# Performance work log

Measured on AMD Instinct MI355X. Metric: run time of the kernel, lower is better.

Reference implementation:

```python
import jax, jax.numpy as jnp
import numpy as np

# Fixed production-scale dims (equal-size graphs -> no ragged padding needed)
B, NPG, C, H, L, FFN, NC = 16, 512, 128, 8, 4, 512, 4
D = C // H          # head dim = 16
T = NPG + 1         # +1 virtual graph token
EPG = 8192          # edges per graph (avg degree 16)
E = B * EPG


def _ln(x, g, b, eps=1e-5):
    m = x.mean(-1, keepdims=True)
    v = ((x - m) ** 2).mean(-1, keepdims=True)
    return (x - m) * jax.lax.rsqrt(v + eps) * g + b


def setup_inputs() -> dict:
    key = jax.random.key(0)
    ks = jax.random.split(key, 24)
    N = B * NPG
    node_feats = jax.random.normal(ks[0], (N, 3), jnp.float32)
    # intra-graph edges: local endpoints + per-graph node offset (matches batch_ptr math)
    local = jax.random.randint(ks[1], (2, B, EPG), 0, NPG)
    offs = (jnp.arange(B) * NPG)[None, :, None]
    edge_index = (local + offs).reshape(2, E)
    edge_attr = jax.random.randint(ks[2], (E,), 0, 10)

    def nrm(k, shape, scale=0.02):
        return jax.random.normal(k, shape, jnp.float32) * scale

    params = {
        "W_node": nrm(ks[3], (3, C), 0.3), "b_node": jnp.zeros((C,), jnp.float32),
        "graph_token": nrm(ks[4], (C,), 1.0),
        "edge_bias_table": nrm(ks[5], (11, H), 0.1).at[0].set(0.0),  # padding_idx=0
        "in_deg_emb": nrm(ks[6], (512, C)).at[0].set(0.0),           # padding_idx=0
        "out_deg_emb": nrm(ks[7], (512, C)).at[0].set(0.0),
        "vnode_bias": nrm(ks[8], (H,), 1.0),
        "Wq": nrm(ks[9], (L, C, C)), "bq": jnp.zeros((L, C), jnp.float32),
        "Wk": nrm(ks[10], (L, C, C)), "bk": jnp.zeros((L, C), jnp.float32),
        "Wv": nrm(ks[11], (L, C, C)), "bv": jnp.zeros((L, C), jnp.float32),
        "Wo": nrm(ks[12], (L, C, C)), "bo": jnp.zeros((L, C), jnp.float32),
        "ln1_g": jnp.ones((L, C), jnp.float32), "ln1_b": jnp.zeros((L, C), jnp.float32),
        "ln2_g": jnp.ones((L, C), jnp.float32), "ln2_b": jnp.zeros((L, C), jnp.float32),
        "W1": nrm(ks[13], (L, C, FFN)), "b1": jnp.zeros((L, FFN), jnp.float32),
        "W2": nrm(ks[14], (L, FFN, C)), "b2": jnp.zeros((L, C), jnp.float32),
        "normf_g": jnp.ones((C,), jnp.float32), "normf_b": jnp.zeros((C,), jnp.float32),
        "Wc1": nrm(ks[15], (C, C // 2)), "bc1": jnp.zeros((C // 2,), jnp.float32),
        "Wc2": nrm(ks[16], (C // 2, NC)), "bc2": jnp.zeros((NC,), jnp.float32),
    }
    return {"node_feats": node_feats, "edge_index": edge_index,
            "edge_attr": edge_attr, "num_graphs": B, **params}


def reference(node_feats, W_node, b_node, graph_token, edge_bias_table,
              in_deg_emb, out_deg_emb, vnode_bias,
              Wq, bq, Wk, bk, Wv, bv, Wo, bo,
              ln1_g, ln1_b, ln2_g, ln2_b, W1, b1, W2, b2,
              normf_g, normf_b, Wc1, bc1, Wc2, bc2,
              edge_index, edge_attr, num_graphs):
    N = node_feats.shape[0]
    npg = N // num_graphs
    t = npg + 1
    src, dst = edge_index[0], edge_index[1]
    # degree encoders (scatter_add of ones == segment_sum)
    in_deg = jnp.clip(jax.ops.segment_sum(jnp.ones_like(dst), dst, num_segments=N), 0, 511)
    out_deg = jnp.clip(jax.ops.segment_sum(jnp.ones_like(src), src, num_segments=N), 0, 511)
    x_enc = node_feats @ W_node + b_node + in_deg_emb[in_deg] + out_deg_emb[out_deg]
    # equal-size graphs with sorted batch ids -> padding loop is a reshape, mask all-False
    x = jnp.concatenate(
        [jnp.broadcast_to(graph_token, (num_graphs, 1, C)),
         x_enc.reshape(num_graphs, npg, C)], axis=1)  # [B, T, C]
    # attention bias: vnode row/col + scattered edge-attr embeddings
    bias = jnp.zeros((num_graphs, H, t, t), jnp.float32)
    bias = bias.at[:, :, 0, :].set(vnode_bias[None, :, None])
    bias = bias.at[:, :, :, 0].set(vnode_bias[None, :, None])
    eb = edge_bias_table[jnp.clip(edge_attr, 0, 9) + 1]  # [E, H]
    g = src // npg
    sl = src - g * npg + 1
    dl = dst - g * npg + 1
    bias = bias.at[g, :, sl, dl].add(eb)  # duplicate edges accumulate (scatter_add)
    scale = 1.0 / np.sqrt(D).astype(np.float32)
    for l in range(L):  # key_padding_mask is all-False here -> masked_fill is a no-op
        h = _ln(x, ln1_g[l], ln1_b[l])
        q = (h @ Wq[l] + bq[l]).reshape(num_graphs, t, H, D)
        k = (h @ Wk[l] + bk[l]).reshape(num_graphs, t, H, D)
        v = (h @ Wv[l] + bv[l]).reshape(num_graphs, t, H, D)
        scores = jnp.einsum('bthd,bshd->bhts', q, k) * scale + bias
        attn = jax.nn.softmax(scores, axis=-1)
        o = jnp.einsum('bhts,bshd->bthd', attn, v).reshape(num_graphs, t, C)
        x = x + o @ Wo[l] + bo[l]
        h2 = _ln(x, ln2_g[l], ln2_b[l])
        x = x + jax.nn.gelu(h2 @ W1[l] + b1[l], approximate=False) @ W2[l] + b2[l]
    x = _ln(x, normf_g, normf_b)
    gr = x[:, 0, :]  # virtual-node readout
    return jax.nn.gelu(gr @ Wc1 + bc1, approximate=False) @ Wc2 + bc2
```

## Files before the change

### kernel.cpp

```cpp
#include <hip/hip_runtime.h>
#include <hip/hip_bf16.h>

#define BB 16
#define NPG 512
#define CC 128
#define HH 8
#define LL 4
#define FFN 512
#define NCLS 4
#define DD 16
#define TT 513
#define EE 131072
#define NNODES 8192
#define ROWS (BB * TT)
#define ECAP 64
#define SP 544
#define BPAD 544

static constexpr size_t XROWS = (size_t)BB * TT;
static constexpr size_t XSZ   = XROWS * CC;
static constexpr size_t VTSZ  = (size_t)BB * HH * DD * SP;
static constexpr size_t BIASSZ = (size_t)BB * HH * 513 * BPAD;

typedef unsigned short ushort_t;
typedef __attribute__((ext_vector_type(8))) short short8;
typedef __attribute__((ext_vector_type(4))) float floatx4;

__device__ __forceinline__ float gelu_exact(float v) {
    return 0.5f * v * (1.0f + erff(v * 0.70710678118654752440f));
}
__device__ __forceinline__ ushort_t f2bf(float f) {
    union { float f; unsigned u; } c; c.f = f;
    unsigned u = c.u;
    return (ushort_t)((u + 0x7FFFu + ((u >> 16) & 1u)) >> 16);
}
__device__ __forceinline__ float bf2f(ushort_t u) {
    union { unsigned u; float f; } c; c.u = ((unsigned)u) << 16; return c.f;
}
__device__ __forceinline__ int swz(int row, int col, int stride) {
    int kb = col >> 3;
    return row * stride + (((kb ^ (row & 7)) << 3) | (col & 7));
}

__device__ __forceinline__ void qkv_stage8(const ushort_t* hs,
                                           const ushort_t* Wtq, const float* bq_,
                                           const ushort_t* Wtk, const float* bk_,
                                           const ushort_t* Wtv, const float* bv_,
                                           ushort_t* qb, ushort_t* kb, ushort_t* vt,
                                           int b, int t0, int wave, int lq, int quad) {
    const short* hsS = (const short*)hs;
    int c = wave * 16 + lq;
    const short* Ws[3] = {(const short*)Wtq, (const short*)Wtk, (const short*)Wtv};
    const float* bs[3] = {bq_, bk_, bv_};
    size_t rB = (size_t)c * CC;

    #pragma unroll
    for (int m = 0; m < 3; ++m) {
        const short* W = Ws[m];
        floatx4 a0 = {0.f,0.f,0.f,0.f};
        #pragma unroll
        for (int k0 = 0; k0 < CC; k0 += 32) {
            short8 af = *(const short8*)(hsS + swz(lq, k0 + quad * 8, 128));
            short8 b0 = *(const short8*)(W + rB + k0 + quad * 8);
            a0 = __builtin_amdgcn_mfma_f32_16x16x32_bf16(af, b0, a0, 0, 0, 0);
        }
        float bv0 = bs[m][c];
        #pragma unroll
        for (int rg = 0; rg < 4; ++rg) {
            int t = t0 + quad * 4 + rg;
            if (t >= TT) continue;
            size_t r = (size_t)b * TT + t;
            float v0 = a0[rg] + bv0;
            if (m == 0) {
                qb[r * CC + c] = f2bf(v0 * 0.25f);
            } else if (m == 1) {
                kb[r * CC + c] = f2bf(v0);
            } else {
                vt[((size_t)(b * HH + wave) * DD + lq) * SP + t] = f2bf(v0);
            }
        }
    }
}

__global__ __launch_bounds__(256) void deg_csr_tr_kernel(const int* __restrict__ ei,
                                                         const int* __restrict__ ea,
                                                         int* __restrict__ deg_in,
                                                         int* __restrict__ deg_out,
                                                         int* __restrict__ cnt,
                                                         int* __restrict__ ebuf,
                                                         const float* __restrict__ Wq,
                                                         const float* __restrict__ Wk,
                                                         const float* __restrict__ Wv,
                                                         const float* __restrict__ Wo,
                                                         const float* __restrict__ W1,
                                                         const float* __restrict__ W2,
                                                         ushort_t* __restrict__ wtqkvo,
                                                         ushort_t* __restrict__ wt1,
                                                         ushort_t* __restrict__ wt2) {
    int bid = blockIdx.x;
    int tid = threadIdx.x;
    if (bid < 512) {
        int e = bid * 256 + tid;
        int src = ei[e], dst = ei[EE + e];
        atomicAdd(&deg_out[src], 1);
        atomicAdd(&deg_in[dst], 1);
        int g = src >> 9;
        int sl = src - (g << 9) + 1;
        int dl = dst - (g << 9) + 1;
        int a = ea[e];
        a = (a < 0) ? 0 : (a > 9 ? 9 : a);
        a += 1;
        int row = g * TT + sl;
        int pos = atomicAdd(&cnt[row], 1);
        if (pos < ECAP) ebuf[(size_t)row * ECAP + pos] = dl | (a << 16);
        return;
    }
    int z = bid - 512;
    const float* src; ushort_t* dst; int K, N, tile;
    if (z < 64) {
        int zz = z >> 2; tile = z & 3;
        int k = zz >> 2, l = zz & 3;
        const float* s4[4] = {Wq, Wk, Wv, Wo};
        src = s4[k] + (size_t)l * CC * CC;
        dst = wtqkvo + (size_t)(k * 4 + l) * 16384;
        K = CC; N = CC;
    } else if (z < 128) {
        int l = (z - 64) >> 4; tile = (z - 64) & 15;
        src = W1 + (size_t)l * CC * FFN;
        dst = wt1 + (size_t)l * 65536;
        K = CC; N = FFN;
    } else {
        int l = (z - 128) >> 4; tile = (z - 128) & 15;
        src = W2 + (size_t)l * FFN * CC;
        dst = wt2 + (size_t)l * 65536;
        K = FFN; N = CC;
    }
    int tilesN = N >> 6;
    int k0 = (tile / tilesN) << 6;
    int n0 = (tile - (tile / tilesN) * tilesN) << 6;
    __shared__ float t[64][65];
    int c = tid & 63, rb = tid >> 6;
    #pragma unroll
    for (int kk = 0; kk < 64; kk += 4)
        t[kk + rb][c] = src[(size_t)(k0 + kk + rb) * N + n0 + c];
    __syncthreads();
    #pragma unroll
    for (int nn = 0; nn < 64; nn += 4)
        dst[(size_t)(n0 + nn + rb) * K + k0 + c] = f2bf(t[c][nn + rb]);
}

__global__ __launch_bounds__(512) void pre_kernel(const float* __restrict__ nf,
                                                  const float* __restrict__ Wn,
                                                  const float* __restrict__ bn,
                                                  const float* __restrict__ gt,
                                                  const float* __restrict__ ide,
                                                  const float* __restrict__ ode,
                                                  const int* __restrict__ deg_in,
                                                  const int* __restrict__ deg_out,
                                                  const float* __restrict__ ln1g_,
                                                  const float* __restrict__ ln1b_,
                                                  const ushort_t* __restrict__ wtqkvo,
                                                  const float* __restrict__ bq_,
                                                  const float* __restrict__ bk_,
                                                  const float* __restrict__ bv_,
                                                  float* __restrict__ x_,
                                                  ushort_t* __restrict__ qb,
                                                  ushort_t* __restrict__ kb,
                                                  ushort_t* __restrict__ vt,
                                                  const int* __restrict__ cnt,
                                                  const int* __restrict__ ebuf,
                                                  const float* __restrict__ ebt,
                                                  ushort_t* __restrict__ bias_d) {
    int bid = blockIdx.x;
    int tid = threadIdx.x;
    __shared__ __align__(16) char parena[17408];

    if (bid >= 528) {
        int z = bid - 528;
        int b = z / 513;
        int sl = z - b * 513;
        float* row8 = (float*)parena;
        for (int i = tid; i < 8 * BPAD / 4; i += 512)
            ((float4*)row8)[i] = make_float4(0.f, 0.f, 0.f, 0.f);
        __syncthreads();
        int crow = b * TT + sl;
        int cn = min(cnt[crow], ECAP);
        int h = tid & 7;
        for (int j = tid >> 3; j < cn; j += 64) {
            int e = ebuf[(size_t)crow * ECAP + j];
            atomicAdd(&row8[h * BPAD + (e & 0xFFFF)], ebt[(e >> 16) * 8 + h]);
        }
        __syncthreads();
        #pragma unroll
        for (int hh = 0; hh < HH; ++hh) {
            size_t base = ((size_t)(b * HH + hh) * 513 + sl) * BPAD;
            for (int s = tid; s < BPAD; s += 512)
                bias_d[base + s] = f2bf(row8[hh * BPAD + s]);
        }
        return;
    }

    int b = bid / 33, qt = bid - b * 33;
    int t0 = qt * 16;
    int wave = tid >> 6, lane = tid & 63, lq = lane & 15, quad = lane >> 4;
    ushort_t* hs = (ushort_t*)parena;
    auto sred = (float (*)[16][2])(parena + 4096);

    int c = wave * 16 + lq;
    float w0[4];
    #pragma unroll
    for (int rg = 0; rg < 4; ++rg) {
        int t = t0 + quad * 4 + rg;
        int tc = min(t, TT - 1);
        float v0;
        if (tc == 0) {
            v0 = gt[c];
        } else {
            int i = b * NPG + tc - 1;
            float f0 = nf[i*3+0], f1 = nf[i*3+1], f2 = nf[i*3+2];
            v0 = bn[c] + f0*Wn[0*CC + c] + f1*Wn[1*CC + c] + f2*Wn[2*CC + c];
            int di = min(deg_in[i], 511);
            int dq = min(deg_out[i], 511);
            v0 += ide[(size_t)di * CC + c] + ode[(size_t)dq * CC + c];
        }
        if (t < TT) x_[((size_t)b * TT + t) * CC + c] = v0;
        w0[rg] = v0;
    }
    #pragma unroll
    for (int rg = 0; rg < 4; ++rg) {
        float s1 = w0[rg];
        float s2 = w0[rg] * w0[rg];
        #pragma unroll
        for (int m = 1; m < 16; m <<= 1) {
            s1 += __shfl_xor(s1, m, 64);
            s2 += __shfl_xor(s2, m, 64);
        }
        if (lq == 0) { sred[wave][quad*4+rg][0] = s1; sred[wave][quad*4+rg][1] = s2; }
    }
    __syncthreads();
    float g0 = ln1g_[c], lb0 = ln1b_[c];
    #pragma unroll
    for (int rg = 0; rg < 4; ++rg) {
        int row = quad * 4 + rg;
        float S1 = 0.f, S2 = 0.f;
        #pragma unroll
        for (int w = 0; w < 8; ++w) { S1 += sred[w][row][0]; S2 += sred[w][row][1]; }
        float mn = S1 * (1.0f/CC);
        float var = S2 * (1.0f/CC) - mn * mn;
        float rs = rsqrtf(var + 1e-5f);
        hs[swz(row, c, 128)] = f2bf((w0[rg] - mn) * rs * g0 + lb0);
    }
    __syncthreads();
    qkv_stage8(hs, wtqkvo, bq_,
               wtqkvo + (size_t)4 * 16384, bk_,
               wtqkvo + (size_t)8 * 16384, bv_,
               qb, kb, vt, b, t0, wave, lq, quad);
}

__global__ __launch_bounds__(512, 4) void layer_kernel(const ushort_t* __restrict__ qbr,
                                                       const ushort_t* __restrict__ kbr,
                                                       const ushort_t* __restrict__ vtr,
                                                       const ushort_t* __restrict__ bias_d,
                                                       const float* __restrict__ vnode,
                                                       const ushort_t* __restrict__ WtO,
                                                       const float* __restrict__ bo_,
                                                       const float* __restrict__ ln2g_,
                                                       const float* __restrict__ ln2b_,
                                                       const ushort_t* __restrict__ Wt1_,
                                                       const float* __restrict__ b1_,
                                                       const ushort_t* __restrict__ Wt2_,
                                                       const float* __restrict__ b2_,
                                                       const float* __restrict__ ln1g_,
                                                       const float* __restrict__ ln1b_,
                                                       const ushort_t* __restrict__ Wtq,
                                                       const float* __restrict__ bq_,
                                                       const ushort_t* __restrict__ Wtk,
                                                       const float* __restrict__ bk_,
                                                       const ushort_t* __restrict__ Wtv,
                                                       const float* __restrict__ bv_,
                                                       const float* __restrict__ nfg,
                                                       const float* __restrict__ nfb,
                                                       const float* __restrict__ Wc1,
                                                       const float* __restrict__ bc1,
                                                       const float* __restrict__ Wc2,
                                                       const float* __restrict__ bc2,
                                                       float* __restrict__ x_,
                                                       ushort_t* __restrict__ qbw,
                                                       ushort_t* __restrict__ kbw,
                                                       ushort_t* __restrict__ vtw,
                                                       float* __restrict__ out,
                                                       int doQKV) {
    int qt = blockIdx.x, b = blockIdx.y;
    int tid = threadIdx.x;
    int wave = tid >> 6, lane = tid & 63, lq = lane & 15, quad = lane >> 4;

    __shared__ __align__(16) char smem[20480];
    ushort_t* hs = (ushort_t*)smem;
    ushort_t* ms = (ushort_t*)(smem + 4096);
    __shared__ __align__(16) ushort_t obs[16 * 128];
    __shared__ float sred[8][16][2];

    {
        int h = wave;
        int qg = qt * 16 + lq;
        int qr = min(qg, TT - 1);
        short8 z8 = {0,0,0,0,0,0,0,0};
        short8 qf = z8;
        if (quad < 2)
            qf = *(const short8*)(qbr + ((size_t)(b * TT + qr)) * CC + h * DD + quad * 8);
        float vn = vnode[h];
        const short* kbS = (const short*)kbr;
        const short* vtS = (const short*)(vtr + (size_t)(b * HH + h) * DD * SP);
        const ushort_t* brow = bias_d + ((size_t)(b * HH + h) * 513 + qr) * BPAD;

        short8 af0c = z8, af1c = z8, vfc;
        {
            int kr0 = min(b * TT + lq, (int)XROWS - 1);
            int kr1 = min(b * TT + 16 + lq, (int)XROWS - 1);
            if (quad < 2) {
                af0c = *(const short8*)(kbS + (size_t)kr0 * CC + h * DD + quad * 8);
                af1c = *(const short8*)(kbS + (size_t)kr1 * CC + h * DD + quad * 8);
            }
            vfc = *(const short8*)(vtS + (size_t)lq * SP + quad * 8);
        }
        uint2 bi0c = *(const uint2*)(brow + quad * 4);
        uint2 bi1c = *(const uint2*)(brow + 16 + quad * 4);

        floatx4 oacc = {0.f, 0.f, 0.f, 0.f};
        float lsum = 0.f;

        for (int sp = 0; sp < 17; ++sp) {
            int spn = sp + 1;
            short8 af0n = z8, af1n = z8, vfn = z8;
            uint2 bi0n = make_uint2(0u, 0u), bi1n = make_uint2(0u, 0u);
            if (spn < 17) {
                int st0 = spn * 2, st1 = st0 + 1;
                int kr0 = min(b * TT + st0 * 16 + lq, (int)XROWS - 1);
                int kr1 = min(b * TT + st1 * 16 + lq, (int)XROWS - 1);
                if (quad < 2) {
                    af0n = *(const short8*)(kbS + (size_t)kr0 * CC + h * DD + quad * 8);
                    af1n = *(const short8*)(kbS + (size_t)kr1 * CC + h * DD + quad * 8);
                }
                vfn = *(const short8*)(vtS + (size_t)lq * SP + spn * 32 + quad * 8);
                bi0n = *(const uint2*)(brow + spn * 32 + quad * 4);
                bi1n = *(const uint2*)(brow + spn * 32 + 16 + quad * 4);
            }
            float vadd = ((sp == 0) & (quad == 0) & (qg > 0)) ? vn : 0.f;

            unsigned pw[2][2];
            #pragma unroll
            for (int t = 0; t < 2; ++t) {
                int st = sp * 2 + t;
                floatx4 cc4 = __builtin_amdgcn_mfma_f32_16x16x32_bf16(
                    t ? af1c : af0c, qf, (floatx4){0.f, 0.f, 0.f, 0.f}, 0, 0, 0);
                uint2 bi = t ? bi1c : bi0c;
                float pr[4];
                #pragma unroll
                for (int rg = 0; rg < 4; ++rg) {
                    int s = st * 16 + quad * 4 + rg;
                    unsigned bw = (rg < 2) ? bi.x : bi.y;
                    float bb = bf2f((rg & 1) ? (ushort_t)(bw >> 16) : (ushort_t)(bw & 0xFFFFu));
                    if (t == 0 && rg == 0) bb += vadd;
                    float p = 0.f;
                    if (s < TT) p = __expf(cc4[rg] + bb);
                    lsum += p;
                    pr[rg] = p;
                }
                pw[t][0] = (unsigned)f2bf(pr[0]) | ((unsigned)f2bf(pr[1]) << 16);
                pw[t][1] = (unsigned)f2bf(pr[2]) | ((unsigned)f2bf(pr[3]) << 16);
            }
            int srcA = lq + (((2 * quad) & 3) << 4);
            int srcB = lq + (((2 * quad + 1) & 3) << 4);
            int a00 = __shfl((int)pw[0][0], srcA, 64);
            int a01 = __shfl((int)pw[0][1], srcA, 64);
            int a10 = __shfl((int)pw[1][0], srcA, 64);
            int a11 = __shfl((int)pw[1][1], srcA, 64);
            int b00 = __shfl((int)pw[0][0], srcB, 64);
            int b01 = __shfl((int)pw[0][1], srcB, 64);
            int b10 = __shfl((int)pw[1][0], srcB, 64);
            int b11 = __shfl((int)pw[1][1], srcB, 64);
            union { int u[4]; short8 s8; } pu;
            bool lo = quad < 2;
            pu.u[0] = lo ? a00 : a10;
            pu.u[1] = lo ? a01 : a11;
            pu.u[2] = lo ? b00 : b10;
            pu.u[3] = lo ? b01 : b11;
            oacc = __builtin_amdgcn_mfma_f32_16x16x32_bf16(vfc, pu.s8, oacc, 0, 0, 0);

            af0c = af0n; af1c = af1n; vfc = vfn; bi0c = bi0n; bi1c = bi1n;
        }

        lsum += __shfl_xor(lsum, 16, 64);
        lsum += __shfl_xor(lsum, 32, 64);
        #pragma unroll
        for (int rg = 0; rg < 4; ++rg)
            obs[swz(lq, h * DD + quad * 4 + rg, 128)] = f2bf(oacc[rg] / lsum);
    }
    __syncthreads();

    int t0 = qt * 16;
    int c = wave * 16 + lq;
    float vv0[4];
    const short* obsS = (const short*)obs;

    {
        const short* W = (const short*)WtO;
        size_t rB = (size_t)c * CC;
        floatx4 a0 = {0.f,0.f,0.f,0.f};
        #pragma unroll
        for (int k0 = 0; k0 < CC; k0 += 32) {
            short8 af = *(const short8*)(obsS + swz(lq, k0 + quad * 8, 128));
            short8 b0 = *(const short8*)(W + rB + k0 + quad * 8);
            a0 = __builtin_amdgcn_mfma_f32_16x16x32_bf16(af, b0, a0, 0, 0, 0);
        }
        float bv0 = bo_[c];
        #pragma unroll
        for (int rg = 0; rg < 4; ++rg) {
            int t = t0 + quad * 4 + rg;
            size_t rc = (size_t)b * TT + min(t, TT - 1);
            vv0[rg] = a0[rg] + bv0 + x_[rc * CC + c];
        }
        #pragma unroll
        for (int rg = 0; rg < 4; ++rg) {
            float s1 = vv0[rg];
            float s2 = vv0[rg] * vv0[rg];
            #pragma unroll
            for (int m = 1; m < 16; m <<= 1) {
                s1 += __shfl_xor(s1, m, 64);
                s2 += __shfl_xor(s2, m, 64);
            }
            if (lq == 0) { sred[wave][quad*4+rg][0] = s1; sred[wave][quad*4+rg][1] = s2; }
        }
        __syncthreads();
        float g0 = ln2g_[c], lb0 = ln2b_[c];
        #pragma unroll
        for (int rg = 0; rg < 4; ++rg) {
            int row = quad * 4 + rg;
            float S1 = 0.f, S2 = 0.f;
            #pragma unroll
            for (int w = 0; w < 8; ++w) { S1 += sred[w][row][0]; S2 += sred[w][row][1]; }
            float mn = S1 * (1.0f/CC);
            float var = S2 * (1.0f/CC) - mn * mn;
            float rs = rsqrtf(var + 1e-5f);
            hs[swz(row, c, 128)] = f2bf((vv0[rg] - mn) * rs * g0 + lb0);
        }
    }
    __syncthreads();

    {
        const short* hsS = (const short*)hs;
        const short* W = (const short*)Wt1_;
        #pragma unroll
        for (int nt = 0; nt < 4; ++nt) {
            int n = wave * 64 + nt * 16;
            size_t rB = (size_t)(n + lq) * CC;
            floatx4 a0 = {0.f,0.f,0.f,0.f};
            #pragma unroll
            for (int k0 = 0; k0 < CC; k0 += 32) {
                short8 af = *(const short8*)(hsS + swz(lq, k0 + quad * 8, 128));
                short8 b0 = *(const short8*)(W + rB + k0 + quad * 8);
                a0 = __builtin_amdgcn_mfma_f32_16x16x32_bf16(af, b0, a0, 0, 0, 0);
            }
            float bb0 = b1_[n + lq];
            #pragma unroll
            for (int rg = 0; rg < 4; ++rg)
                ms[swz(quad * 4 + rg, n + lq, 512)] = f2bf(gelu_exact(a0[rg] + bb0));
        }
    }
    __syncthreads();

    float w0[4];
    {
        const short* msS = (const short*)ms;
        const short* W = (const short*)Wt2_;
        size_t rB = (size_t)c * FFN;
        floatx4 a0 = {0.f,0.f,0.f,0.f};
        #pragma unroll 8
        for (int k0 = 0; k0 < FFN; k0 += 32) {
            short8 af = *(const short8*)(msS + swz(lq, k0 + quad * 8, 512));
            short8 b0 = *(const short8*)(W + rB + k0 + quad * 8);
            a0 = __builtin_amdgcn_mfma_f32_16x16x32_bf16(af, b0, a0, 0, 0, 0);
        }
        float bv0 = b2_[c];
        #pragma unroll
        for (int rg = 0; rg < 4; ++rg) {
            int t = t0 + quad * 4 + rg;
            w0[rg] = a0[rg] + bv0 + vv0[rg];
            if (t < TT) x_[((size_t)b * TT + t) * CC + c] = w0[rg];
        }
    }

    if (doQKV) {
        #pragma unroll
        for (int rg = 0; rg < 4; ++rg) {
            float s1 = w0[rg];
            float s2 = w0[rg] * w0[rg];
            #pragma unroll
            for (int m = 1; m < 16; m <<= 1) {
                s1 += __shfl_xor(s1, m, 64);
                s2 += __shfl_xor(s2, m, 64);
            }
            if (lq == 0) { sred[wave][quad*4+rg][0] = s1; sred[wave][quad*4+rg][1] = s2; }
        }
        __syncthreads();
        float g0 = ln1g_[c], lb0 = ln1b_[c];
        #pragma unroll
        for (int rg = 0; rg < 4; ++rg) {
            int row = quad * 4 + rg;
            float S1 = 0.f, S2 = 0.f;
            #pragma unroll
            for (int w = 0; w < 8; ++w) { S1 += sred[w][row][0]; S2 += sred[w][row][1]; }
            float mn = S1 * (1.0f/CC);
            float var = S2 * (1.0f/CC) - mn * mn;
            float rs = rsqrtf(var + 1e-5f);
            hs[swz(row, c, 128)] = f2bf((w0[rg] - mn) * rs * g0 + lb0);
        }
        __syncthreads();
        qkv_stage8(hs, Wtq, bq_, Wtk, bk_, Wtv, bv_, qbw, kbw, vtw, b, t0, wave, lq, quad);
        return;
    }

    if (qt != 0) return;

    __syncthreads();
    float* hrow = (float*)ms;
    float* xfs  = hrow + CC;
    float* c1s  = xfs + CC;
    float* red  = c1s + 64;
    if (quad == 0) hrow[c] = w0[0];
    __syncthreads();

    {
        int ct = tid;
        float v = 0.f, s1 = 0.f, s2 = 0.f;
        if (ct < CC) { v = hrow[ct]; s1 = v; s2 = v * v; }
        #pragma unroll
        for (int m = 32; m >= 1; m >>= 1) {
            s1 += __shfl_xor(s1, m, 64);
            s2 += __shfl_xor(s2, m, 64);
        }
        int w = ct >> 6;
        if (ct < CC && (ct & 63) == 0) { red[w*2] = s1; red[w*2+1] = s2; }
        __syncthreads();
        if (ct < CC) {
            float S1 = red[0] + red[2], S2 = red[1] + red[3];
            float mn = S1 * (1.0f/CC);
            float var = S2 * (1.0f/CC) - mn * mn;
            float rs = rsqrtf(var + 1e-5f);
            xfs[ct] = (v - mn) * rs * nfg[ct] + nfb[ct];
        }
        __syncthreads();
        if (ct < 64) {
            float acc = bc1[ct];
            #pragma unroll 4
            for (int k = 0; k < CC; ++k) acc = fmaf(xfs[k], Wc1[(size_t)k * 64 + ct], acc);
            c1s[ct] = gelu_exact(acc);
        }
        __syncthreads();
        if (ct < NCLS) {
            float acc = bc2[ct];
            #pragma unroll 4
            for (int j = 0; j < 64; ++j) acc = fmaf(c1s[j], Wc2[(size_t)j * NCLS + ct], acc);
            out[(size_t)b * NCLS + ct] = acc;
        }
    }
}

extern "C" void kernel_launch(void* const* d_in, const int* in_sizes, int n_in,
                              void* d_out, int out_size, void* d_ws, size_t ws_size,
                              hipStream_t stream) {
    const float* node_feats = (const float*)d_in[0];
    const int*   edge_index = (const int*)d_in[1];
    const int*   edge_attr  = (const int*)d_in[2];
    const float* W_node  = (const float*)d_in[4];
    const float* b_node  = (const float*)d_in[5];
    const float* g_token = (const float*)d_in[6];
    const float* ebt     = (const float*)d_in[7];
    const float* ide     = (const float*)d_in[8];
    const float* ode     = (const float*)d_in[9];
    const float* vnode   = (const float*)d_in[10];
    const float* Wq = (const float*)d_in[11];
    const float* bq = (const float*)d_in[12];
    const float* Wk = (const float*)d_in[13];
    const float* bk = (const float*)d_in[14];
    const float* Wv = (const float*)d_in[15];
    const float* bv = (const float*)d_in[16];
    const float* Wo = (const float*)d_in[17];
    const float* bo = (const float*)d_in[18];
    const float* ln1g = (const float*)d_in[19];
    const float* ln1b = (const float*)d_in[20];
    const float* ln2g = (const float*)d_in[21];
    const float* ln2b = (const float*)d_in[22];
    const float* W1 = (const float*)d_in[23];
    const float* b1 = (const float*)d_in[24];
    const float* W2 = (const float*)d_in[25];
    const float* b2 = (const float*)d_in[26];
    const float* nfg = (const float*)d_in[27];
    const float* nfb = (const float*)d_in[28];
    const float* Wc1 = (const float*)d_in[29];
    const float* bc1 = (const float*)d_in[30];
    const float* Wc2 = (const float*)d_in[31];
    const float* bc2 = (const float*)d_in[32];
    float* out = (float*)d_out;

    char* base = (char*)d_ws;
    float* x      = (float*)base;     base += XSZ * 4;
    ushort_t* qb0 = (ushort_t*)base;  base += XSZ * 2;
    ushort_t* kb0 = (ushort_t*)base;  base += XSZ * 2;
    ushort_t* vt0 = (ushort_t*)base;  base += VTSZ * 2;
    ushort_t* qb1 = (ushort_t*)base;  base += XSZ * 2;
    ushort_t* kb1 = (ushort_t*)base;  base += XSZ * 2;
    ushort_t* vt1 = (ushort_t*)base;  base += VTSZ * 2;
    ushort_t* wtqkvo = (ushort_t*)base; base += (size_t)16 * 16384 * 2;
    ushort_t* wt1 = (ushort_t*)base;  base += (size_t)4 * 65536 * 2;
    ushort_t* wt2 = (ushort_t*)base;  base += (size_t)4 * 65536 * 2;
    ushort_t* bias_d = (ushort_t*)base; base += BIASSZ * 2;
    int* deg_in  = (int*)base;        base += NNODES * 4;
    int* deg_out = (int*)base;        base += NNODES * 4;
    int* cnt     = (int*)base;        base += (size_t)ROWS * 4;
    int* ebuf    = (int*)base;        base += (size_t)ROWS * ECAP * 4;

    ushort_t* qbs[2] = {qb0, qb1};
    ushort_t* kbs[2] = {kb0, kb1};
    ushort_t* vts[2] = {vt0, vt1};

    hipMemsetAsync(deg_in, 0, (size_t)(2 * NNODES + ROWS) * 4, stream);
    deg_csr_tr_kernel<<<512 + 192, 256, 0, stream>>>(
        edge_index, edge_attr, deg_in, deg_out, cnt, ebuf,
        Wq, Wk, Wv, Wo, W1, W2, wtqkvo, wt1, wt2);

    pre_kernel<<<528 + 8208, 512, 0, stream>>>(
        node_feats, W_node, b_node, g_token, ide, ode, deg_in, deg_out,
        ln1g, ln1b, wtqkvo, bq, bk, bv, x, qb0, kb0, vt0,
        cnt, ebuf, ebt, bias_d);

    for (int l = 0; l < LL; ++l) {
        int rd = l & 1, wr = rd ^ 1;
        int ln = (l + 1) % LL;
        layer_kernel<<<dim3(33, BB), 512, 0, stream>>>(
            qbs[rd], kbs[rd], vts[rd], bias_d, vnode,
            wtqkvo + (size_t)(12 + l)*16384, bo + l*CC,
            ln2g + l*CC, ln2b + l*CC,
            wt1 + (size_t)l*65536, b1 + l*FFN,
            wt2 + (size_t)l*65536, b2 + l*CC,
            ln1g + ln*CC, ln1b + ln*CC,
            wtqkvo + (size_t)(0 + ln)*16384, bq + ln*CC,
            wtqkvo + (size_t)(4 + ln)*16384, bk + ln*CC,
            wtqkvo + (size_t)(8 + ln)*16384, bv + ln*CC,
            nfg, nfb, Wc1, bc1, Wc2, bc2,
            x, qbs[wr], kbs[wr], vts[wr], out,
            (l < LL-1) ? 1 : 0);
    }
}
```

Measured before the change: 464.8 us.

## Build attention bias on the fly from per-row edge lists instead of dense bias

Drops the dense bf16 bias tensor (B*H*513*544) that pre_kernel materialized and each layer re-read. Each layer_kernel block now loads the per-query-row edge lists and the edge bias table into shared memory. For each 64-column window it scatters those edges into a per-wave LDS strip with atomicAdd before computing the softmax. This removes a large global write plus four full reads of the bias, at the cost of repeating the scatter work in every layer, extra LDS use (which may limit occupancy) and LDS atomics inside the inner attention loop.

```diff
diff --git a/kernel.cpp b/kernel.cpp
--- a/kernel.cpp
+++ b/kernel.cpp
@@ -15,12 +15,11 @@
 #define ROWS (BB * TT)
 #define ECAP 64
 #define SP 544
-#define BPAD 544
+#define ESTR 68
 
 static constexpr size_t XROWS = (size_t)BB * TT;
 static constexpr size_t XSZ   = XROWS * CC;
 static constexpr size_t VTSZ  = (size_t)BB * HH * DD * SP;
-static constexpr size_t BIASSZ = (size_t)BB * HH * 513 * BPAD;
 
 typedef unsigned short ushort_t;
 typedef __attribute__((ext_vector_type(8))) short short8;
@@ -33,9 +32,6 @@
     union { float f; unsigned u; } c; c.f = f;
     unsigned u = c.u;
     return (ushort_t)((u + 0x7FFFu + ((u >> 16) & 1u)) >> 16);
-}
-__device__ __forceinline__ float bf2f(ushort_t u) {
-    union { unsigned u; float f; } c; c.u = ((unsigned)u) << 16; return c.f;
 }
 __device__ __forceinline__ int swz(int row, int col, int stride) {
     int kb = col >> 3;
@@ -166,45 +162,15 @@
                                                   float* __restrict__ x_,
                                                   ushort_t* __restrict__ qb,
                                                   ushort_t* __restrict__ kb,
-                                                  ushort_t* __restrict__ vt,
-                                                  const int* __restrict__ cnt,
-                                                  const int* __restrict__ ebuf,
-                                                  const float* __restrict__ ebt,
-                                                  ushort_t* __restrict__ bias_d) {
+                                                  ushort_t* __restrict__ vt) {
     int bid = blockIdx.x;
     int tid = threadIdx.x;
-    __shared__ __align__(16) char parena[17408];
-
-    if (bid >= 528) {
-        int z = bid - 528;
-        int b = z / 513;
-        int sl = z - b * 513;
-        float* row8 = (float*)parena;
-        for (int i = tid; i < 8 * BPAD / 4; i += 512)
-            ((float4*)row8)[i] = make_float4(0.f, 0.f, 0.f, 0.f);
-        __syncthreads();
-        int crow = b * TT + sl;
-        int cn = min(cnt[crow], ECAP);
-        int h = tid & 7;
-        for (int j = tid >> 3; j < cn; j += 64) {
-            int e = ebuf[(size_t)crow * ECAP + j];
-            atomicAdd(&row8[h * BPAD + (e & 0xFFFF)], ebt[(e >> 16) * 8 + h]);
-        }
-        __syncthreads();
-        #pragma unroll
-        for (int hh = 0; hh < HH; ++hh) {
-            size_t base = ((size_t)(b * HH + hh) * 513 + sl) * BPAD;
-            for (int s = tid; s < BPAD; s += 512)
-                bias_d[base + s] = f2bf(row8[hh * BPAD + s]);
-        }
-        return;
-    }
-
     int b = bid / 33, qt = bid - b * 33;
     int t0 = qt * 16;
     int wave = tid >> 6, lane = tid & 63, lq = lane & 15, quad = lane >> 4;
-    ushort_t* hs = (ushort_t*)parena;
-    auto sred = (float (*)[16][2])(parena + 4096);
+
+    __shared__ ushort_t hs[16 * 128];
+    __shared__ float sred[8][16][2];
 
     int c = wave * 16 + lq;
     float w0[4];
@@ -260,7 +226,9 @@
 __global__ __launch_bounds__(512, 4) void layer_kernel(const ushort_t* __restrict__ qbr,
                                                        const ushort_t* __restrict__ kbr,
                                                        const ushort_t* __restrict__ vtr,
-                                                       const ushort_t* __restrict__ bias_d,
+                                                       const int* __restrict__ cnt,
+                                                       const int* __restrict__ ebuf,
+                                                       const float* __restrict__ ebt,
                                                        const float* __restrict__ vnode,
                                                        const ushort_t* __restrict__ WtO,
                                                        const float* __restrict__ bo_,
@@ -294,11 +262,28 @@
     int tid = threadIdx.x;
     int wave = tid >> 6, lane = tid & 63, lq = lane & 15, quad = lane >> 4;
 
-    __shared__ __align__(16) char smem[20480];
-    ushort_t* hs = (ushort_t*)smem;
-    ushort_t* ms = (ushort_t*)(smem + 4096);
+    __shared__ __align__(16) char arena[40960];
+    float* strips = (float*)arena;
+    int*   elist  = (int*)(arena + 34816);
+    float* ebt_s  = (float*)(arena + 34816 + 4352);
+    ushort_t* hs = (ushort_t*)arena;
+    ushort_t* ms = (ushort_t*)(arena + 4096);
     __shared__ __align__(16) ushort_t obs[16 * 128];
     __shared__ float sred[8][16][2];
+    __shared__ int cn_s[16];
+
+    {
+        int r = tid >> 5, j2 = (tid & 31) * 2;
+        int qrow = qt * 16 + r;
+        bool rv = (qrow >= 1) && (qrow < TT);
+        size_t crow = (size_t)b * TT + (rv ? qrow : 0);
+        if ((tid & 31) == 0) cn_s[r] = rv ? min(cnt[crow], ECAP) : 0;
+        int2 ee = *(const int2*)(ebuf + crow * ECAP + j2);
+        elist[r * ESTR + j2]     = ee.x;
+        elist[r * ESTR + j2 + 1] = ee.y;
+        if (tid < 88) ebt_s[tid] = ebt[tid];
+    }
+    __syncthreads();
 
     {
         int h = wave;
@@ -311,7 +296,8 @@
         float vn = vnode[h];
         const short* kbS = (const short*)kbr;
         const short* vtS = (const short*)(vtr + (size_t)(b * HH + h) * DD * SP);
-        const ushort_t* brow = bias_d + ((size_t)(b * HH + h) * 513 + qr) * BPAD;
+        float* strip = strips + wave * (16 * ESTR);
+        int cn = cn_s[lq];
 
         short8 af0c = z8, af1c = z8, vfc;
         {
@@ -323,8 +309,6 @@
             }
             vfc = *(const short8*)(vtS + (size_t)lq * SP + quad * 8);
         }
-        uint2 bi0c = *(const uint2*)(brow + quad * 4);
-        uint2 bi1c = *(const uint2*)(brow + 16 + quad * 4);
 
         floatx4 oacc = {0.f, 0.f, 0.f, 0.f};
         float lsum = 0.f;
@@ -332,7 +316,6 @@
         for (int sp = 0; sp < 17; ++sp) {
             int spn = sp + 1;
             short8 af0n = z8, af1n = z8, vfn = z8;
-            uint2 bi0n = make_uint2(0u, 0u), bi1n = make_uint2(0u, 0u);
             if (spn < 17) {
                 int st0 = spn * 2, st1 = st0 + 1;
                 int kr0 = min(b * TT + st0 * 16 + lq, (int)XROWS - 1);
@@ -342,10 +325,30 @@
                     af1n = *(const short8*)(kbS + (size_t)kr1 * CC + h * DD + quad * 8);
                 }
                 vfn = *(const short8*)(vtS + (size_t)lq * SP + spn * 32 + quad * 8);
-                bi0n = *(const uint2*)(brow + spn * 32 + quad * 4);
-                bi1n = *(const uint2*)(brow + spn * 32 + 16 + quad * 4);
-            }
+            }
+
+            if (!(sp & 1)) {
+                int w0 = sp * 32;
+                #pragma unroll
+                for (int k = 0; k < 5; ++k) {
+                    int idx = lane + k * 64;
+                    if (idx < 16 * ESTR / 4)
+                        ((float4*)strip)[idx] = make_float4(0.f, 0.f, 0.f, 0.f);
+                }
+                asm volatile("s_waitcnt lgkmcnt(0)" ::: "memory");
+                for (int j = quad; j < cn; j += 4) {
+                    int e = elist[lq * ESTR + j];
+                    int rel = (e & 0xFFFF) - w0;
+                    if ((unsigned)rel < 64u)
+                        atomicAdd(&strip[lq * ESTR + rel], ebt_s[(e >> 16) * 8 + h]);
+                }
+                asm volatile("s_waitcnt lgkmcnt(0)" ::: "memory");
+            }
+
             float vadd = ((sp == 0) & (quad == 0) & (qg > 0)) ? vn : 0.f;
+            int roff = lq * ESTR + (sp & 1) * 32 + quad * 4;
+            float4 bia = *(const float4*)&strip[roff];
+            float4 bib = *(const float4*)&strip[roff + 16];
 
             unsigned pw[2][2];
             #pragma unroll
@@ -353,13 +356,13 @@
                 int st = sp * 2 + t;
                 floatx4 cc4 = __builtin_amdgcn_mfma_f32_16x16x32_bf16(
                     t ? af1c : af0c, qf, (floatx4){0.f, 0.f, 0.f, 0.f}, 0, 0, 0);
-                uint2 bi = t ? bi1c : bi0c;
+                float4 bi = t ? bib : bia;
+                float biv[4] = {bi.x, bi.y, bi.z, bi.w};
                 float pr[4];
                 #pragma unroll
                 for (int rg = 0; rg < 4; ++rg) {
                     int s = st * 16 + quad * 4 + rg;
-                    unsigned bw = (rg < 2) ? bi.x : bi.y;
-                    float bb = bf2f((rg & 1) ? (ushort_t)(bw >> 16) : (ushort_t)(bw & 0xFFFFu));
+                    float bb = biv[rg];
                     if (t == 0 && rg == 0) bb += vadd;
                     float p = 0.f;
                     if (s < TT) p = __expf(cc4[rg] + bb);
@@ -387,7 +390,7 @@
             pu.u[3] = lo ? b01 : b11;
             oacc = __builtin_amdgcn_mfma_f32_16x16x32_bf16(vfc, pu.s8, oacc, 0, 0, 0);
 
-            af0c = af0n; af1c = af1n; vfc = vfn; bi0c = bi0n; bi1c = bi1n;
+            af0c = af0n; af1c = af1n; vfc = vfn;
         }
 
         lsum += __shfl_xor(lsum, 16, 64);
@@ -614,7 +617,6 @@
     ushort_t* wtqkvo = (ushort_t*)base; base += (size_t)16 * 16384 * 2;
     ushort_t* wt1 = (ushort_t*)base;  base += (size_t)4 * 65536 * 2;
     ushort_t* wt2 = (ushort_t*)base;  base += (size_t)4 * 65536 * 2;
-    ushort_t* bias_d = (ushort_t*)base; base += BIASSZ * 2;
     int* deg_in  = (int*)base;        base += NNODES * 4;
     int* deg_out = (int*)base;        base += NNODES * 4;
     int* cnt     = (int*)base;        base += (size_t)ROWS * 4;
@@ -629,16 +631,15 @@
         edge_index, edge_attr, deg_in, deg_out, cnt, ebuf,
         Wq, Wk, Wv, Wo, W1, W2, wtqkvo, wt1, wt2);
 
-    pre_kernel<<<528 + 8208, 512, 0, stream>>>(
+    pre_kernel<<<528, 512, 0, stream>>>(
         node_feats, W_node, b_node, g_token, ide, ode, deg_in, deg_out,
-        ln1g, ln1b, wtqkvo, bq, bk, bv, x, qb0, kb0, vt0,
-        cnt, ebuf, ebt, bias_d);
+        ln1g, ln1b, wtqkvo, bq, bk, bv, x, qb0, kb0, vt0);
 
     for (int l = 0; l < LL; ++l) {
         int rd = l & 1, wr = rd ^ 1;
         int ln = (l + 1) % LL;
         layer_kernel<<<dim3(33, BB), 512, 0, stream>>>(
-            qbs[rd], kbs[rd], vts[rd], bias_d, vnode,
+            qbs[rd], kbs[rd], vts[rd], cnt, ebuf, ebt, vnode,
             wtqkvo + (size_t)(12 + l)*16384, bo + l*CC,
             ln2g + l*CC, ln2b + l*CC,
             wt1 + (size_t)l*65536, b1 + l*FFN,
```

New measurement: 465.0 us. Within noise of the previous version (+0.0%).
